# Performance work log

Measured on AMD Instinct MI355X. Metric: run time of the kernel, lower is better.

## Reference

```python
import jax, jax.numpy as jnp
import numpy as np

NUM_Q_HEADS = 32
NUM_KV_HEADS = 8
HEAD_DIM = 128
HIDDEN = 4096
EPS = 1e-6
ROPE_THETA = 1e6


def _rmsnorm(t, w):
    # per-head RMSNorm over last dim (head_dim), as in skip_rmsnorm with residual=None
    var = jnp.mean(t * t, axis=-1, keepdims=True)
    return t * jax.lax.rsqrt(var + EPS) * w


def _rotate_half(t):
    h = t.shape[-1] // 2
    return jnp.concatenate([-t[..., h:], t[..., :h]], axis=-1)


def setup_inputs() -> dict:
    key = jax.random.key(0)
    ks = jax.random.split(key, 4)
    B, S = 2, 1024
    x = jax.random.normal(ks[0], (B, S, HIDDEN), jnp.float32)
    q_proj_w = jax.random.normal(ks[1], (HIDDEN, NUM_Q_HEADS * HEAD_DIM), jnp.float32) * 0.02
    kv_proj_w = jax.random.normal(ks[2], (HIDDEN, 2 * NUM_KV_HEADS * HEAD_DIM), jnp.float32) * 0.02
    o_proj_w = jax.random.normal(ks[3], (NUM_Q_HEADS * HEAD_DIM, HIDDEN), jnp.float32) * 0.02
    q_norm_w = jnp.ones((HEAD_DIM,), jnp.float32)
    k_norm_w = jnp.ones((HEAD_DIM,), jnp.float32)
    # real rotate-half RoPE tables, shape [S, head_dim]
    inv_freq = 1.0 / (ROPE_THETA ** (jnp.arange(0, HEAD_DIM, 2, dtype=jnp.float32) / HEAD_DIM))
    freqs = jnp.arange(S, dtype=jnp.float32)[:, None] * inv_freq[None, :]  # [S, hd/2]
    emb = jnp.concatenate([freqs, freqs], axis=-1)  # [S, hd]
    cos, sin = jnp.cos(emb), jnp.sin(emb)
    kv_buffer = jnp.zeros((16384, 2 * NUM_KV_HEADS, HEAD_DIM), jnp.float32)
    cur_select_index = jnp.arange(B * S, dtype=jnp.int32)
    return {"x": x, "q_proj_w": q_proj_w, "kv_proj_w": kv_proj_w, "o_proj_w": o_proj_w,
            "q_norm_w": q_norm_w, "k_norm_w": k_norm_w, "cos": cos, "sin": sin,
            "kv_buffer": kv_buffer, "cur_select_index": cur_select_index}


def reference(x, q_proj_w, kv_proj_w, o_proj_w, q_norm_w, k_norm_w, cos, sin, kv_buffer, cur_select_index):
    B, S, _ = x.shape
    T = B * S
    xf = x.reshape(T, HIDDEN)
    # projections (weights stored as [in, out])
    xq = (xf @ q_proj_w).reshape(T, NUM_Q_HEADS, HEAD_DIM)
    xkv = xf @ kv_proj_w
    xk = xkv[:, : NUM_KV_HEADS * HEAD_DIM].reshape(T, NUM_KV_HEADS, HEAD_DIM)
    xv = xkv[:, NUM_KV_HEADS * HEAD_DIM:].reshape(T, NUM_KV_HEADS, HEAD_DIM)
    # per-head RMSNorm (Qwen3 q/k norm)
    xq = _rmsnorm(xq, q_norm_w)
    xk = _rmsnorm(xk, k_norm_w)
    # RoPE (cos/sin are [S, hd], tiled over batch, broadcast over heads)
    cos_t = jnp.tile(cos, (B, 1))[:, None, :]  # [T,1,hd]
    sin_t = jnp.tile(sin, (B, 1))[:, None, :]
    xq = xq * cos_t + _rotate_half(xq) * sin_t
    xk = xk * cos_t + _rotate_half(xk) * sin_t
    # paged KV-cache scatter update (update_kv_buffer)
    combined_kv = jnp.concatenate([xk, xv], axis=1)  # [T, 2*Hk, hd]
    buf = kv_buffer.at[cur_select_index].set(combined_kv)
    # ragged causal flash attention (equal per-request lengths here), GQA expand
    rep = NUM_Q_HEADS // NUM_KV_HEADS
    q = xq.reshape(B, S, NUM_Q_HEADS, HEAD_DIM)
    k = jnp.repeat(xk.reshape(B, S, NUM_KV_HEADS, HEAD_DIM), rep, axis=2)
    v = jnp.repeat(xv.reshape(B, S, NUM_KV_HEADS, HEAD_DIM), rep, axis=2)
    scale = HEAD_DIM ** -0.5
    scores = jnp.einsum('bqhd,bkhd->bhqk', q, k) * scale  # [B,H,S,S]
    causal = jnp.tril(jnp.ones((S, S), bool))
    scores = jnp.where(causal[None, None], scores, jnp.float32(-1e30))
    p = jax.nn.softmax(scores, axis=-1)
    attn = jnp.einsum('bhqk,bkhd->bqhd', p, v).reshape(B, S, NUM_Q_HEADS * HEAD_DIM)
    out = attn @ o_proj_w  # [B,S,hidden]
    return out, buf
```

## Files before the change

kernel.cpp:

```cpp
#include <hip/hip_runtime.h>

typedef float fx4 __attribute__((ext_vector_type(4)));
typedef short s16x4 __attribute__((ext_vector_type(4)));
typedef short s16x8 __attribute__((ext_vector_type(8)));
typedef __bf16 bf16x8 __attribute__((ext_vector_type(8)));

__device__ __forceinline__ short f2bf(float f) {
  unsigned u = __builtin_bit_cast(unsigned, f);
  u += 0x7fffu + ((u >> 16) & 1u);
  return (short)(u >> 16);
}

__device__ __forceinline__ bf16x8 ld8(const short* p) {
  s16x8 v = *(const s16x8*)p;
  return __builtin_bit_cast(bf16x8, v);
}

__device__ __forceinline__ void gld16(const void* g, void* l) {
  __builtin_amdgcn_global_load_lds(
      (const __attribute__((address_space(1))) unsigned*)g,
      (__attribute__((address_space(3))) unsigned*)l, 16, 0, 0);
}

__global__ __launch_bounds__(256) void cvt_k(const float* __restrict__ in,
                                             short* __restrict__ out) {
  int i = (blockIdx.x * 256 + threadIdx.x) * 8;
  fx4 a = *(const fx4*)(in + i);
  fx4 b = *(const fx4*)(in + i + 4);
  s16x8 w;
  w[0] = f2bf(a[0]); w[1] = f2bf(a[1]); w[2] = f2bf(a[2]); w[3] = f2bf(a[3]);
  w[4] = f2bf(b[0]); w[5] = f2bf(b[1]); w[6] = f2bf(b[2]); w[7] = f2bf(b[3]);
  *(s16x8*)(out + i) = w;
}

__global__ __launch_bounds__(256) void tr_k(const float* __restrict__ in,
    short* __restrict__ out, int K, int N) {
  __shared__ short T[64][72];
  const int ktiles = K >> 6;
  const int tk0 = (blockIdx.x % ktiles) << 6;
  const int tn0 = (blockIdx.x / ktiles) << 6;
  const int tid = threadIdx.x;
  #pragma unroll
  for (int i = 0; i < 4; ++i) {
    int idx = i * 256 + tid;
    int k = idx >> 4, n4 = (idx & 15) << 2;
    fx4 v = *(const fx4*)(in + (size_t)(tk0 + k) * N + tn0 + n4);
    #pragma unroll
    for (int j = 0; j < 4; ++j) T[n4 + j][k] = f2bf(v[j]);
  }
  __syncthreads();
  #pragma unroll
  for (int i = 0; i < 2; ++i) {
    int idx = i * 256 + tid;
    int n = idx >> 3, k8 = (idx & 7) << 3;
    *(s16x8*)(out + (size_t)(tn0 + n) * K + tk0 + k8) = *(const s16x8*)&T[n][k8];
  }
}

__global__ __launch_bounds__(256) void gemm_k(const short* __restrict__ A,
    const short* __restrict__ Bt, float* __restrict__ Cp, int N, int K) {
  __shared__ short As[2][128 * 64];
  __shared__ short Bs[2][128 * 64];
  const int tiles_n = N >> 7;
  const int tm = blockIdx.x / tiles_n, tn = blockIdx.x % tiles_n;
  const int tid = threadIdx.x;
  const int lane = tid & 63, wv = tid >> 6;
  const int wr = (wv >> 1) << 6, wc = (wv & 1) << 6;
  const int r0 = tm << 7, c0 = tn << 7;
  const int lrow = lane & 15, lg = lane >> 4;
  const int srow = tid >> 3, sch = tid & 7;
  fx4 acc[4][4] = {};

  auto stage = [&](int buf, int k0) {
    #pragma unroll
    for (int i = 0; i < 4; ++i) {
      int row = (i << 5) + srow;
      int gk = ((sch ^ (row & 7)) << 3);
      gld16(A + (size_t)(r0 + row) * K + k0 + gk, &As[buf][(i * 256 + wv * 64) * 8]);
    }
    #pragma unroll
    for (int i = 0; i < 4; ++i) {
      int row = (i << 5) + srow;
      int gk = ((sch ^ (row & 7)) << 3);
      gld16(Bt + (size_t)(c0 + row) * K + k0 + gk, &Bs[buf][(i * 256 + wv * 64) * 8]);
    }
  };

  const int nt = K >> 6;
  stage(0, 0);
  __syncthreads();
  int cur = 0;
  for (int t = 0; t < nt; ++t) {
    if (t + 1 < nt) stage(cur ^ 1, (t + 1) << 6);
    bf16x8 af[4][2], bfr[4][2];
    #pragma unroll
    for (int m = 0; m < 4; ++m) {
      int row = wr + m * 16 + lrow;
      #pragma unroll
      for (int h = 0; h < 2; ++h)
        af[m][h] = ld8(&As[cur][row * 64 + ((((h << 2) + lg) ^ (row & 7)) << 3)]);
    }
    #pragma unroll
    for (int n = 0; n < 4; ++n) {
      int row = wc + n * 16 + lrow;
      #pragma unroll
      for (int h = 0; h < 2; ++h)
        bfr[n][h] = ld8(&Bs[cur][row * 64 + ((((h << 2) + lg) ^ (row & 7)) << 3)]);
    }
    __builtin_amdgcn_s_setprio(1);
    #pragma unroll
    for (int m = 0; m < 4; ++m)
      #pragma unroll
      for (int n = 0; n < 4; ++n) {
        acc[m][n] = __builtin_amdgcn_mfma_f32_16x16x32_bf16(af[m][0], bfr[n][0], acc[m][n], 0, 0, 0);
        acc[m][n] = __builtin_amdgcn_mfma_f32_16x16x32_bf16(af[m][1], bfr[n][1], acc[m][n], 0, 0, 0);
      }
    __builtin_amdgcn_s_setprio(0);
    __syncthreads();
    cur ^= 1;
  }
  const int g4 = lg << 2;
  #pragma unroll
  for (int m = 0; m < 4; ++m)
    #pragma unroll
    for (int n = 0; n < 4; ++n)
      #pragma unroll
      for (int j = 0; j < 4; ++j) {
        int row = r0 + wr + m * 16 + g4 + j;
        int col = c0 + wc + n * 16 + lrow;
        Cp[(size_t)row * N + col] = acc[m][n][j];
      }
}

__global__ __launch_bounds__(256) void nr_k(const float* __restrict__ xqkv,
    const float* __restrict__ qnw, const float* __restrict__ knw,
    const float* __restrict__ cosb, const float* __restrict__ sinb,
    const int* __restrict__ idx,
    short* __restrict__ qb, short* __restrict__ kbp, short* __restrict__ vbp,
    float* __restrict__ bufo) {
  int rid = blockIdx.x * 4 + (threadIdx.x >> 6);
  int l = threadIdx.x & 63;
  int type, t, h;
  if (rid < 65536)      { type = 0; t = rid >> 5; h = rid & 31; }
  else if (rid < 81920) { type = 1; int r = rid - 65536; t = r >> 3; h = r & 7; }
  else                  { type = 2; int r = rid - 81920; t = r >> 3; h = r & 7; }
  int s = t & 1023;
  const float* src = xqkv + (size_t)t * 6144 +
                     ((type == 0) ? h * 128 : (type == 1) ? 4096 + h * 128
                                                          : 5120 + h * 128);
  float e0 = src[l], e1 = src[l + 64];
  float out0, out1;
  if (type < 2) {
    float ss = e0 * e0 + e1 * e1;
    #pragma unroll
    for (int off = 1; off < 64; off <<= 1) ss += __shfl_xor(ss, off);
    float r = rsqrtf(ss * (1.0f / 128.0f) + 1e-6f);
    const float* nw = (type == 0) ? qnw : knw;
    float n0 = e0 * r * nw[l], n1 = e1 * r * nw[l + 64];
    float c0 = cosb[s * 128 + l], c1 = cosb[s * 128 + 64 + l];
    float s0 = sinb[s * 128 + l], s1 = sinb[s * 128 + 64 + l];
    out0 = n0 * c0 - n1 * s0;
    out1 = n1 * c1 + n0 * s1;
  } else { out0 = e0; out1 = e1; }
  if (type == 0) {
    short* d = qb + (size_t)t * 4096 + h * 128;
    d[l] = f2bf(out0); d[l + 64] = f2bf(out1);
  } else {
    int br = idx[t];
    float* bd = bufo + (size_t)br * 2048 + (type == 1 ? 0 : 1024) + h * 128;
    bd[l] = out0; bd[l + 64] = out1;
    short* d = (type == 1) ? kbp + (size_t)t * 1024 + h * 128
                           : vbp + (size_t)t * 1024 + h * 128;
    d[l] = f2bf(out0); d[l + 64] = f2bf(out1);
  }
}

#define KLD 136
#define VLD 72
#define PLD 72

__global__ __launch_bounds__(256) void attn_k(const short* __restrict__ qb,
    const short* __restrict__ kbp, const short* __restrict__ vbp,
    short* __restrict__ ob) {
  __shared__ short Ks[64 * KLD];
  __shared__ short Vs[128 * VLD];
  __shared__ short Ps[4][16 * PLD];
  const int bid = blockIdx.x;
  const int qt = bid & 15, h = (bid >> 4) & 31, b = bid >> 9;
  const int kvh = h >> 2;
  const int tid = threadIdx.x, lane = tid & 63, w = tid >> 6;
  const int lrow = lane & 15, lg = lane >> 4, lk = lg << 3;
  const int q0 = qt << 6;
  const float SC2 = 0.088388347648318447f * 1.4426950408889634f;

  bf16x8 qf[4];
  {
    const short* qp = qb + ((size_t)(b * 1024 + q0 + w * 16 + lrow) * 32 + h) * 128 + lk;
    #pragma unroll
    for (int kb4 = 0; kb4 < 4; ++kb4) qf[kb4] = ld8(qp + kb4 * 32);
  }
  float m[4], lsum[4];
  fx4 acc[8] = {};
  #pragma unroll
  for (int j = 0; j < 4; ++j) { m[j] = -3.0e38f; lsum[j] = 0.f; }

  for (int kt = 0; kt <= qt; ++kt) {
    const int kv0 = kt << 6;
    #pragma unroll
    for (int it = 0; it < 4; ++it) {
      int idx = it * 256 + tid;
      int r = idx >> 4, d8 = (idx & 15) << 3;
      size_t base = ((size_t)(b * 1024 + kv0 + r) * 8 + kvh) * 128 + d8;
      *(s16x8*)&Ks[r * KLD + d8] = *(const s16x8*)(kbp + base);
      s16x8 vv = *(const s16x8*)(vbp + base);
      int swz = ((d8 >> 3) & 7) << 3;
      #pragma unroll
      for (int j = 0; j < 8; ++j)
        Vs[(d8 + j) * VLD + (r ^ swz)] = vv[j];
    }
    __syncthreads();
    fx4 sf[4];
    #pragma unroll
    for (int nc = 0; nc < 4; ++nc) {
      fx4 z = {0.f, 0.f, 0.f, 0.f};
      sf[nc] = z;
      #pragma unroll
      for (int kb4 = 0; kb4 < 4; ++kb4) {
        bf16x8 kf = ld8(&Ks[(nc * 16 + lrow) * KLD + kb4 * 32 + lk]);
        sf[nc] = __builtin_amdgcn_mfma_f32_16x16x32_bf16(qf[kb4], kf, sf[nc], 0, 0, 0);
      }
    }
    if (kt == qt) {
      #pragma unroll
      for (int nc = 0; nc < 4; ++nc)
        #pragma unroll
        for (int j = 0; j < 4; ++j) {
          int qr = q0 + w * 16 + (lg << 2) + j;
          int kc = kv0 + nc * 16 + lrow;
          if (kc > qr) sf[nc][j] = -3.0e38f;
        }
    }
    float pm[4];
    #pragma unroll
    for (int j = 0; j < 4; ++j) pm[j] = -3.0e38f;
    #pragma unroll
    for (int nc = 0; nc < 4; ++nc)
      #pragma unroll
      for (int j = 0; j < 4; ++j) pm[j] = fmaxf(pm[j], sf[nc][j]);
    #pragma unroll
    for (int j = 0; j < 4; ++j) {
      pm[j] = fmaxf(pm[j], __shfl_xor(pm[j], 1));
      pm[j] = fmaxf(pm[j], __shfl_xor(pm[j], 2));
      pm[j] = fmaxf(pm[j], __shfl_xor(pm[j], 4));
      pm[j] = fmaxf(pm[j], __shfl_xor(pm[j], 8));
    }
    float alpha[4], rs[4];
    #pragma unroll
    for (int j = 0; j < 4; ++j) {
      float mn = fmaxf(m[j], pm[j]);
      alpha[j] = exp2f((m[j] - mn) * SC2);
      m[j] = mn;
      rs[j] = 0.f;
    }
    #pragma unroll
    for (int nc = 0; nc < 4; ++nc)
      #pragma unroll
      for (int j = 0; j < 4; ++j) {
        float p = exp2f((sf[nc][j] - m[j]) * SC2);
        rs[j] += p;
        Ps[w][((lg << 2) + j) * PLD + nc * 16 + lrow] = f2bf(p);
      }
    #pragma unroll
    for (int j = 0; j < 4; ++j) {
      rs[j] += __shfl_xor(rs[j], 1);
      rs[j] += __shfl_xor(rs[j], 2);
      rs[j] += __shfl_xor(rs[j], 4);
      rs[j] += __shfl_xor(rs[j], 8);
      lsum[j] = lsum[j] * alpha[j] + rs[j];
    }
    #pragma unroll
    for (int dg = 0; dg < 8; ++dg)
      #pragma unroll
      for (int j = 0; j < 4; ++j) acc[dg][j] *= alpha[j];
    #pragma unroll
    for (int kb2 = 0; kb2 < 2; ++kb2) {
      bf16x8 pf = ld8(&Ps[w][lrow * PLD + kb2 * 32 + lk]);
      #pragma unroll
      for (int dg = 0; dg < 8; ++dg) {
        int d = dg * 16 + lrow;
        int kvs = (kb2 * 32 + lk) ^ (((d >> 3) & 7) << 3);
        bf16x8 vf = ld8(&Vs[d * VLD + kvs]);
        acc[dg] = __builtin_amdgcn_mfma_f32_16x16x32_bf16(pf, vf, acc[dg], 0, 0, 0);
      }
    }
    __syncthreads();
  }
  #pragma unroll
  for (int j = 0; j < 4; ++j) {
    float rl = 1.0f / lsum[j];
    int t = b * 1024 + q0 + w * 16 + (lg << 2) + j;
    short* op = ob + ((size_t)t * 32 + h) * 128;
    #pragma unroll
    for (int dg = 0; dg < 8; ++dg)
      op[dg * 16 + lrow] = f2bf(acc[dg][j] * rl);
  }
}

extern "C" void kernel_launch(void* const* d_in, const int* in_sizes, int n_in,
                              void* d_out, int out_size, void* d_ws, size_t ws_size,
                              hipStream_t stream) {
  (void)in_sizes; (void)n_in; (void)out_size; (void)ws_size;
  const float* x    = (const float*)d_in[0];
  const float* qw   = (const float*)d_in[1];
  const float* kvw  = (const float*)d_in[2];
  const float* ow   = (const float*)d_in[3];
  const float* qnw  = (const float*)d_in[4];
  const float* knw  = (const float*)d_in[5];
  const float* cosb = (const float*)d_in[6];
  const float* sinb = (const float*)d_in[7];
  const float* kvbf = (const float*)d_in[8];
  const int*   idx  = (const int*)d_in[9];

  float* outp = (float*)d_out;
  float* bufp = outp + (size_t)2048 * 4096;

  char* ws = (char*)d_ws;
  float* xqkv = (float*)ws;
  short* qb   = (short*)(ws + (size_t)2048 * 6144 * 4);
  short* kbp  = (short*)((char*)qb + (size_t)2048 * 4096 * 2);
  short* vbp  = (short*)((char*)kbp + (size_t)2048 * 1024 * 2);
  short* attnb = (short*)xqkv;
  short* owt   = (short*)((char*)xqkv + (size_t)2048 * 4096 * 2);

  short* wqkvt = (short*)bufp;
  short* xb    = (short*)((char*)bufp + (size_t)6144 * 4096 * 2);

  cvt_k<<<dim3(4096), dim3(256), 0, stream>>>(x, xb);
  tr_k<<<dim3(64 * 64), dim3(256), 0, stream>>>(qw, wqkvt, 4096, 4096);
  tr_k<<<dim3(64 * 32), dim3(256), 0, stream>>>(kvw, wqkvt + (size_t)4096 * 4096, 4096, 2048);
  gemm_k<<<dim3(16 * 48), dim3(256), 0, stream>>>(xb, wqkvt, xqkv, 6144, 4096);
  hipMemcpyAsync(bufp + (size_t)2048 * 2048, kvbf + (size_t)2048 * 2048,
                 (size_t)(16384 - 2048) * 2048 * 4, hipMemcpyDeviceToDevice, stream);
  nr_k<<<dim3(98304 / 4), dim3(256), 0, stream>>>(xqkv, qnw, knw, cosb, sinb, idx,
                                                  qb, kbp, vbp, bufp);
  tr_k<<<dim3(64 * 64), dim3(256), 0, stream>>>(ow, owt, 4096, 4096);
  attn_k<<<dim3(2 * 32 * 16), dim3(256), 0, stream>>>(qb, kbp, vbp, attnb);
  gemm_k<<<dim3(16 * 32), dim3(256), 0, stream>>>(attnb, owt, outp, 4096, 4096);
}
```

Before: 441.9 us.

## Pre-transpose V and read K/V fragments directly from global memory in attention

Adds a small kernel that transposes V into a per-(batch, kv-head) [d, t] layout in the workspace, reusing the o_proj transposed-weight slot. The attention kernel is reordered to run before the o_proj weight transpose so it can use that slot. The attention kernel no longer stages K and V through LDS with block-wide barriers; each wave loads its MFMA operand fragments straight from global memory (through L2), which removes the shared-memory transposes and the two syncthreads per KV tile. The trade-off is redundant global loads across the four waves and across the q heads that share a kv head, plus an extra launch and a V round trip through memory.

```diff
diff --git a/kernel.cpp b/kernel.cpp
--- a/kernel.cpp
+++ b/kernel.cpp
@@ -54,6 +54,33 @@
     int idx = i * 256 + tid;
     int n = idx >> 3, k8 = (idx & 7) << 3;
     *(s16x8*)(out + (size_t)(tn0 + n) * K + tk0 + k8) = *(const s16x8*)&T[n][k8];
+  }
+}
+
+__global__ __launch_bounds__(256) void vtr_k(const short* __restrict__ vbp,
+                                             short* __restrict__ vbt) {
+  __shared__ short T[64][72];
+  const int tile = blockIdx.x & 31;
+  const int tt = tile & 15, dt = tile >> 4;
+  const int bk = blockIdx.x >> 5;
+  const int b = bk >> 3, kvh = bk & 7;
+  const int t0 = tt << 6, d0 = dt << 6;
+  const int tid = threadIdx.x;
+  #pragma unroll
+  for (int i = 0; i < 2; ++i) {
+    int idx = i * 256 + tid;
+    int r = idx >> 3, c8 = (idx & 7) << 3;
+    s16x8 v = *(const s16x8*)(vbp + (size_t)(b * 1024 + t0 + r) * 1024 + kvh * 128 + d0 + c8);
+    #pragma unroll
+    for (int j = 0; j < 8; ++j) T[c8 + j][r] = v[j];
+  }
+  __syncthreads();
+  #pragma unroll
+  for (int i = 0; i < 2; ++i) {
+    int idx = i * 256 + tid;
+    int r = idx >> 3, c8 = (idx & 7) << 3;
+    *(s16x8*)(vbt + ((size_t)(b * 8 + kvh) * 128 + d0 + r) * 1024 + t0 + c8) =
+        *(const s16x8*)&T[r][c8];
   }
 }
 
@@ -175,15 +202,11 @@
   }
 }
 
-#define KLD 136
-#define VLD 72
 #define PLD 72
 
 __global__ __launch_bounds__(256) void attn_k(const short* __restrict__ qb,
-    const short* __restrict__ kbp, const short* __restrict__ vbp,
+    const short* __restrict__ kbp, const short* __restrict__ vbt,
     short* __restrict__ ob) {
-  __shared__ short Ks[64 * KLD];
-  __shared__ short Vs[128 * VLD];
   __shared__ short Ps[4][16 * PLD];
   const int bid = blockIdx.x;
   const int qt = bid & 15, h = (bid >> 4) & 31, b = bid >> 9;
@@ -199,6 +222,9 @@
     #pragma unroll
     for (int kb4 = 0; kb4 < 4; ++kb4) qf[kb4] = ld8(qp + kb4 * 32);
   }
+  const short* kb_base = kbp + (size_t)(b * 1024) * 1024 + kvh * 128;
+  const short* vt_base = vbt + (size_t)(b * 8 + kvh) * 128 * 1024;
+
   float m[4], lsum[4];
   fx4 acc[8] = {};
   #pragma unroll
@@ -206,28 +232,24 @@
 
   for (int kt = 0; kt <= qt; ++kt) {
     const int kv0 = kt << 6;
-    #pragma unroll
-    for (int it = 0; it < 4; ++it) {
-      int idx = it * 256 + tid;
-      int r = idx >> 4, d8 = (idx & 15) << 3;
-      size_t base = ((size_t)(b * 1024 + kv0 + r) * 8 + kvh) * 128 + d8;
-      *(s16x8*)&Ks[r * KLD + d8] = *(const s16x8*)(kbp + base);
-      s16x8 vv = *(const s16x8*)(vbp + base);
-      int swz = ((d8 >> 3) & 7) << 3;
-      #pragma unroll
-      for (int j = 0; j < 8; ++j)
-        Vs[(d8 + j) * VLD + (r ^ swz)] = vv[j];
-    }
-    __syncthreads();
     fx4 sf[4];
     #pragma unroll
-    for (int nc = 0; nc < 4; ++nc) {
-      fx4 z = {0.f, 0.f, 0.f, 0.f};
-      sf[nc] = z;
-      #pragma unroll
-      for (int kb4 = 0; kb4 < 4; ++kb4) {
-        bf16x8 kf = ld8(&Ks[(nc * 16 + lrow) * KLD + kb4 * 32 + lk]);
-        sf[nc] = __builtin_amdgcn_mfma_f32_16x16x32_bf16(qf[kb4], kf, sf[nc], 0, 0, 0);
+    for (int np = 0; np < 2; ++np) {
+      bf16x8 kf[2][4];
+      #pragma unroll
+      for (int u = 0; u < 2; ++u)
+        #pragma unroll
+        for (int kb4 = 0; kb4 < 4; ++kb4)
+          kf[u][kb4] = ld8(kb_base + (size_t)(kv0 + (np * 2 + u) * 16 + lrow) * 1024
+                           + kb4 * 32 + lk);
+      #pragma unroll
+      for (int u = 0; u < 2; ++u) {
+        fx4 z = {0.f, 0.f, 0.f, 0.f};
+        fx4 s = z;
+        #pragma unroll
+        for (int kb4 = 0; kb4 < 4; ++kb4)
+          s = __builtin_amdgcn_mfma_f32_16x16x32_bf16(qf[kb4], kf[u][kb4], s, 0, 0, 0);
+        sf[np * 2 + u] = s;
       }
     }
     if (kt == qt) {
@@ -285,15 +307,14 @@
     #pragma unroll
     for (int kb2 = 0; kb2 < 2; ++kb2) {
       bf16x8 pf = ld8(&Ps[w][lrow * PLD + kb2 * 32 + lk]);
-      #pragma unroll
-      for (int dg = 0; dg < 8; ++dg) {
-        int d = dg * 16 + lrow;
-        int kvs = (kb2 * 32 + lk) ^ (((d >> 3) & 7) << 3);
-        bf16x8 vf = ld8(&Vs[d * VLD + kvs]);
-        acc[dg] = __builtin_amdgcn_mfma_f32_16x16x32_bf16(pf, vf, acc[dg], 0, 0, 0);
-      }
-    }
-    __syncthreads();
+      bf16x8 vf[8];
+      #pragma unroll
+      for (int dg = 0; dg < 8; ++dg)
+        vf[dg] = ld8(vt_base + (size_t)(dg * 16 + lrow) * 1024 + kv0 + kb2 * 32 + lk);
+      #pragma unroll
+      for (int dg = 0; dg < 8; ++dg)
+        acc[dg] = __builtin_amdgcn_mfma_f32_16x16x32_bf16(pf, vf[dg], acc[dg], 0, 0, 0);
+    }
   }
   #pragma unroll
   for (int j = 0; j < 4; ++j) {
@@ -331,6 +352,7 @@
   short* vbp  = (short*)((char*)kbp + (size_t)2048 * 1024 * 2);
   short* attnb = (short*)xqkv;
   short* owt   = (short*)((char*)xqkv + (size_t)2048 * 4096 * 2);
+  short* vbt   = owt;
 
   short* wqkvt = (short*)bufp;
   short* xb    = (short*)((char*)bufp + (size_t)6144 * 4096 * 2);
@@ -343,7 +365,8 @@
                  (size_t)(16384 - 2048) * 2048 * 4, hipMemcpyDeviceToDevice, stream);
   nr_k<<<dim3(98304 / 4), dim3(256), 0, stream>>>(xqkv, qnw, knw, cosb, sinb, idx,
                                                   qb, kbp, vbp, bufp);
+  vtr_k<<<dim3(512), dim3(256), 0, stream>>>(vbp, vbt);
+  attn_k<<<dim3(2 * 32 * 16), dim3(256), 0, stream>>>(qb, kbp, vbt, attnb);
   tr_k<<<dim3(64 * 64), dim3(256), 0, stream>>>(ow, owt, 4096, 4096);
-  attn_k<<<dim3(2 * 32 * 16), dim3(256), 0, stream>>>(qb, kbp, vbp, attnb);
   gemm_k<<<dim3(16 * 32), dim3(256), 0, stream>>>(attnb, owt, outp, 4096, 4096);
 }
```

Result: slower. 566.8 us (+28.3%).

## Prefetch next K/V tile into registers and schedule longest query tiles first

Applied to the files above, without the earlier changes.

The attention kernel now issues global loads for the next K/V tile into registers before computing on the current tile, then writes them to LDS after the compute, so global latency overlaps the MFMA work. Block-to-query-tile mapping is reversed so causal tiles with the most KV iterations are launched first, which should reduce tail imbalance. The prefetch adds register pressure from 8 extra 16-byte values per thread, which could lower occupancy, and each iteration now has an extra barrier.

```diff
diff --git a/kernel.cpp b/kernel.cpp
--- a/kernel.cpp
+++ b/kernel.cpp
@@ -186,7 +186,7 @@
   __shared__ short Vs[128 * VLD];
   __shared__ short Ps[4][16 * PLD];
   const int bid = blockIdx.x;
-  const int qt = bid & 15, h = (bid >> 4) & 31, b = bid >> 9;
+  const int qt = 15 - (bid & 15), h = (bid >> 4) & 31, b = bid >> 9;
   const int kvh = h >> 2;
   const int tid = threadIdx.x, lane = tid & 63, w = tid >> 6;
   const int lrow = lane & 15, lg = lane >> 4, lk = lg << 3;
@@ -199,26 +199,42 @@
     #pragma unroll
     for (int kb4 = 0; kb4 < 4; ++kb4) qf[kb4] = ld8(qp + kb4 * 32);
   }
+
+  const int sr = tid >> 4, sd8 = (tid & 15) << 3;
+  s16x8 kreg[4], vreg[4];
+  auto ldkv = [&](int kv0) {
+    #pragma unroll
+    for (int it = 0; it < 4; ++it) {
+      int r = (it << 4) + sr;
+      size_t base = ((size_t)(b * 1024 + kv0 + r) * 8 + kvh) * 128 + sd8;
+      kreg[it] = *(const s16x8*)(kbp + base);
+      vreg[it] = *(const s16x8*)(vbp + base);
+    }
+  };
+  auto wrkv = [&]() {
+    #pragma unroll
+    for (int it = 0; it < 4; ++it) {
+      int r = (it << 4) + sr;
+      *(s16x8*)&Ks[r * KLD + sd8] = kreg[it];
+      int swz = ((sd8 >> 3) & 7) << 3;
+      #pragma unroll
+      for (int j = 0; j < 8; ++j)
+        Vs[(sd8 + j) * VLD + (r ^ swz)] = vreg[it][j];
+    }
+  };
+
   float m[4], lsum[4];
   fx4 acc[8] = {};
   #pragma unroll
   for (int j = 0; j < 4; ++j) { m[j] = -3.0e38f; lsum[j] = 0.f; }
 
+  ldkv(0);
+  wrkv();
+  __syncthreads();
+
   for (int kt = 0; kt <= qt; ++kt) {
     const int kv0 = kt << 6;
-    #pragma unroll
-    for (int it = 0; it < 4; ++it) {
-      int idx = it * 256 + tid;
-      int r = idx >> 4, d8 = (idx & 15) << 3;
-      size_t base = ((size_t)(b * 1024 + kv0 + r) * 8 + kvh) * 128 + d8;
-      *(s16x8*)&Ks[r * KLD + d8] = *(const s16x8*)(kbp + base);
-      s16x8 vv = *(const s16x8*)(vbp + base);
-      int swz = ((d8 >> 3) & 7) << 3;
-      #pragma unroll
-      for (int j = 0; j < 8; ++j)
-        Vs[(d8 + j) * VLD + (r ^ swz)] = vv[j];
-    }
-    __syncthreads();
+    if (kt < qt) ldkv((kt + 1) << 6);
     fx4 sf[4];
     #pragma unroll
     for (int nc = 0; nc < 4; ++nc) {
@@ -294,6 +310,10 @@
       }
     }
     __syncthreads();
+    if (kt < qt) {
+      wrkv();
+      __syncthreads();
+    }
   }
   #pragma unroll
   for (int j = 0; j < 4; ++j) {
```

New measurement: 437.2 us. No clear change (-1.1%).
